# Kernel tuning notes

Measured on AMD Instinct MI355X. Metric: run time of the kernel, lower is better.

Reference implementation:

```python
import jax, jax.numpy as jnp
import numpy as np

B, D, H, W = 16, 96, 96, 96
NUM_POINTS = 4096
THRESH = 0.5
CH = [3, 64, 128, 256, 512]   # shared-MLP channel progression (3 mlp layers + global_dim)
GROUPS = 8
EPS = 1e-5
HEAD_HIDDEN = 128


def setup_inputs() -> dict:
    key = jax.random.key(0)
    ks = jax.random.split(key, 8)
    inp = {"volume": jax.random.uniform(ks[0], (B, 1, D, H, W), jnp.float32)}
    for i in range(4):
        # Conv1d(kernel=1, no bias) weight (out, in); kaiming normal fan_out -> std=sqrt(2/out)
        inp[f"w{i+1}"] = jax.random.normal(ks[1 + i], (CH[i + 1], CH[i]), jnp.float32) * np.sqrt(2.0 / CH[i + 1]).astype(np.float32)
        inp[f"gn{i+1}_w"] = jnp.ones((CH[i + 1],), jnp.float32)
        inp[f"gn{i+1}_b"] = jnp.zeros((CH[i + 1],), jnp.float32)
    inp["fc1_w"] = jax.random.normal(ks[5], (HEAD_HIDDEN, CH[-1]), jnp.float32) * np.sqrt(2.0 / HEAD_HIDDEN).astype(np.float32)
    inp["fc1_b"] = jnp.zeros((HEAD_HIDDEN,), jnp.float32)
    inp["fc2_w"] = jax.random.normal(ks[6], (1, HEAD_HIDDEN), jnp.float32) * np.sqrt(2.0).astype(np.float32)
    inp["fc2_b"] = jnp.zeros((1,), jnp.float32)
    return inp


def volume_to_points(volume):
    """Batched, jit-safe version of volume_to_pointcloud (eval mode: linspace sampling)."""
    b, _, d, h, w = volume.shape
    mask = (volume[:, 0] > THRESH).reshape(b, -1)              # (B, D*H*W)
    n = mask.sum(axis=1)                                        # (B,) foreground counts
    # Stable argsort on ~mask puts foreground flat-indices first, in ascending order
    # == torch nonzero() ordering (row-major over D,H,W).
    order = jnp.argsort(jnp.logical_not(mask), axis=1, stable=True)  # (B, D*H*W)
    p = jnp.arange(NUM_POINTS)
    n_f = n.astype(jnp.float32)[:, None]
    # torch.linspace(0, n-1, P).long(): truncation toward zero
    lin = (p[None, :].astype(jnp.float32) * (n_f - 1.0) / (NUM_POINTS - 1)).astype(jnp.int32)
    lin = jnp.clip(lin, 0, jnp.maximum(n[:, None] - 1, 0))
    wrap = p[None, :] % jnp.maximum(n[:, None], 1)              # n < P fallback
    idx = jnp.where(n[:, None] >= NUM_POINTS, lin, wrap)        # (B, P)
    flat = jnp.take_along_axis(order, idx, axis=1)              # (B, P) flat voxel indices
    dd = flat // (h * w)
    hh = (flat // w) % h
    ww = flat % w
    coords = jnp.stack([dd, hh, ww], axis=1).astype(jnp.float32)  # (B, 3, P)
    scale = jnp.array([max(d - 1, 1), max(h - 1, 1), max(w - 1, 1)], jnp.float32)
    pts = coords / scale[None, :, None] * 2.0 - 1.0
    return jnp.where((n > 0)[:, None, None], pts, 0.0)


def group_norm(x, gamma, beta):
    b, c, npts = x.shape
    xg = x.reshape(b, GROUPS, c // GROUPS, npts)
    mu = xg.mean(axis=(2, 3), keepdims=True)
    var = xg.var(axis=(2, 3), keepdims=True)
    xn = ((xg - mu) * jax.lax.rsqrt(var + EPS)).reshape(b, c, npts)
    return xn * gamma[None, :, None] + beta[None, :, None]


def reference(volume, w1, gn1_w, gn1_b, w2, gn2_w, gn2_b, w3, gn3_w, gn3_b,
              w4, gn4_w, gn4_b, fc1_w, fc1_b, fc2_w, fc2_b):
    x = volume_to_points(volume)                                 # (B, 3, P)
    for cw, gw, gb in ((w1, gn1_w, gn1_b), (w2, gn2_w, gn2_b),
                       (w3, gn3_w, gn3_b), (w4, gn4_w, gn4_b)):
        x = jax.nn.relu(group_norm(jnp.einsum('oc,bcn->bon', cw, x), gw, gb))
    g = x.max(axis=2)                                            # (B, 512) global max-pool
    hdn = jax.nn.relu(g @ fc1_w.T + fc1_b)                       # dropout is identity in eval
    logits = (hdn @ fc2_w.T + fc2_b)[:, 0]                       # squeeze(-1) -> (B,)
    return logits
```

## Files before the change

### kernel.cpp

```cpp
#include <hip/hip_runtime.h>
#include <hip/hip_bf16.h>

#define NB 16
#define VOX 884736
#define NPTS 4096
#define CHUNK 1024
#define NCHUNK 864

typedef _Float16 f16x8 __attribute__((ext_vector_type(8)));
typedef _Float16 f16x4 __attribute__((ext_vector_type(4)));
typedef float f32x4 __attribute__((ext_vector_type(4)));


__global__ __launch_bounds__(256) void count_kernel(const float* __restrict__ vol,
                                                    int* __restrict__ counts,
                                                    unsigned long long* __restrict__ bits) {
    int blk = blockIdx.x;
    const float4* v4 = (const float4*)(vol + (size_t)blk * CHUNK);
    float4 v = v4[threadIdx.x];
    int nib = (v.x > 0.5f) | ((v.y > 0.5f) << 1) | ((v.z > 0.5f) << 2) | ((v.w > 0.5f) << 3);
    __shared__ unsigned char nibs[256];
    nibs[threadIdx.x] = (unsigned char)nib;
    int cnt = __popc(nib);
    for (int off = 32; off; off >>= 1) cnt += __shfl_down(cnt, off, 64);
    __shared__ int s[4];
    if ((threadIdx.x & 63) == 0) s[threadIdx.x >> 6] = cnt;
    __syncthreads();
    if (threadIdx.x < 16) {
        unsigned long long wd = 0;
        #pragma unroll
        for (int i = 0; i < 16; i++)
            wd |= (unsigned long long)nibs[threadIdx.x * 16 + i] << (4 * i);
        bits[(size_t)blk * 16 + threadIdx.x] = wd;
    }
    if (threadIdx.x == 0) counts[blk] = s[0] + s[1] + s[2] + s[3];
}

__global__ __launch_bounds__(1024) void scan_kernel(const int* __restrict__ counts,
                                                    int* __restrict__ prefix,
                                                    int* __restrict__ totals) {
    __shared__ int s[1024];
    int b = blockIdx.x, t = threadIdx.x;
    int v = (t < NCHUNK) ? counts[b * NCHUNK + t] : 0;
    s[t] = v;
    __syncthreads();
    for (int off = 1; off < 1024; off <<= 1) {
        int x = (t >= off) ? s[t - off] : 0;
        __syncthreads();
        s[t] += x;
        __syncthreads();
    }
    if (t < NCHUNK) prefix[b * NCHUNK + t] = s[t] - v;
    if (t == NCHUNK - 1) totals[b] = s[t];
}


__global__ __launch_bounds__(256) void points_kernel(const unsigned long long* __restrict__ bits,
                                                     const int* __restrict__ prefix,
                                                     const int* __restrict__ totals,
                                                     const float* __restrict__ w1,
                                                     float* __restrict__ pts,
                                                     float* __restrict__ pstat1) {
    int b = blockIdx.x >> 4;
    int pc = blockIdx.x & 15;
    int p = pc * 256 + threadIdx.x;
    __shared__ int spref[NCHUNK];
    __shared__ float sw1[192];
    for (int i = threadIdx.x; i < NCHUNK; i += 256) spref[i] = prefix[b * NCHUNK + i];
    if (threadIdx.x < 192) sw1[threadIdx.x] = w1[threadIdx.x];
    __syncthreads();
    int n = totals[b];
    float px = 0.f, py = 0.f, pz = 0.f;
    if (n > 0) {
        int k;
        if (n >= NPTS) {
            float t = (float)p * ((float)n - 1.0f);
            t = t / 4095.0f;
            k = (int)t;
            if (k > n - 1) k = n - 1;
            if (k < 0) k = 0;
        } else {
            k = p % n;
        }
        int lo = 0, hi = NCHUNK - 1;
        while (lo < hi) {
            int mid = (lo + hi + 1) >> 1;
            if (spref[mid] <= k) lo = mid; else hi = mid - 1;
        }
        int rr = k - spref[lo];
        const unsigned long long* wb = bits + ((size_t)b * NCHUNK + lo) * 16;
        unsigned long long chosen = 0;
        int wordidx = 0;
        bool found = false;
        #pragma unroll
        for (int w = 0; w < 16; w++) {
            unsigned long long m = wb[w];
            int pcnt = __popcll(m);
            bool take = (!found) && (rr < pcnt);
            if (take) { chosen = m; wordidx = w; found = true; }
            if (!found) rr -= pcnt;
        }
        int pos = 0;
        unsigned long long m64 = chosen;
        int c = __popcll(m64 & 0xFFFFFFFFull);
        if (rr >= c) { pos = 32; rr -= c; m64 >>= 32; }
        unsigned mm = (unsigned)m64;
        c = __popc(mm & 0xFFFFu); if (rr >= c) { pos += 16; rr -= c; mm >>= 16; }
        c = __popc(mm & 0xFFu);   if (rr >= c) { pos += 8;  rr -= c; mm >>= 8; }
        c = __popc(mm & 0xFu);    if (rr >= c) { pos += 4;  rr -= c; mm >>= 4; }
        c = __popc(mm & 0x3u);    if (rr >= c) { pos += 2;  rr -= c; mm >>= 2; }
        c = mm & 1u;              if (rr >= c) { pos += 1; }
        int flat = lo * CHUNK + wordidx * 64 + pos;
        int dd = flat / 9216;
        int rem = flat - dd * 9216;
        int hh = rem / 96;
        int ww = rem - hh * 96;
        px = (float)dd / 95.0f * 2.0f - 1.0f;
        py = (float)hh / 95.0f * 2.0f - 1.0f;
        pz = (float)ww / 95.0f * 2.0f - 1.0f;
    }
    pts[((size_t)b * 3 + 0) * NPTS + p] = px;
    pts[((size_t)b * 3 + 1) * NPTS + p] = py;
    pts[((size_t)b * 3 + 2) * NPTS + p] = pz;
    float s[8] = {}, q[8] = {};
    #pragma unroll
    for (int o = 0; o < 64; o++) {
        float a = sw1[o * 3 + 0] * px + sw1[o * 3 + 1] * py + sw1[o * 3 + 2] * pz;
        s[o >> 3] += a;
        q[o >> 3] += a * a;
    }
    __shared__ float red[4][8][2];
    int wv = threadIdx.x >> 6;
    #pragma unroll
    for (int g = 0; g < 8; g++) {
        float S = s[g], Q = q[g];
        for (int off = 32; off; off >>= 1) {
            S += __shfl_down(S, off, 64);
            Q += __shfl_down(Q, off, 64);
        }
        if ((threadIdx.x & 63) == 0) { red[wv][g][0] = S; red[wv][g][1] = Q; }
    }
    __syncthreads();
    if (threadIdx.x < 8) {
        int g = threadIdx.x;
        float S = red[0][g][0] + red[1][g][0] + red[2][g][0] + red[3][g][0];
        float Q = red[0][g][1] + red[1][g][1] + red[2][g][1] + red[3][g][1];
        float* d = pstat1 + (((size_t)(b * 8 + g)) * 16 + pc) * 2;
        d[0] = S; d[1] = Q;
    }
}

__global__ __launch_bounds__(64) void gn_finalize1(const float* __restrict__ pstat,
                                                   const float* __restrict__ gamma,
                                                   const float* __restrict__ beta,
                                                   float* __restrict__ scale,
                                                   float* __restrict__ shift) {
    int b = blockIdx.x >> 3, g = blockIdx.x & 7;
    const float* base = pstat + (size_t)(b * 8 + g) * 32;
    float S = 0.f, Q = 0.f;
    if (threadIdx.x < 16) { S = base[threadIdx.x * 2]; Q = base[threadIdx.x * 2 + 1]; }
    for (int off = 8; off; off >>= 1) {
        S += __shfl_down(S, off, 64);
        Q += __shfl_down(Q, off, 64);
    }
    __shared__ float ms[2];
    if (threadIdx.x == 0) {
        float inv = 1.0f / (8.0f * 4096.0f);
        float mu = S * inv;
        float var = Q * inv - mu * mu;
        if (var < 0.f) var = 0.f;
        ms[0] = mu; ms[1] = rsqrtf(var + 1e-5f);
    }
    __syncthreads();
    if (threadIdx.x < 8) {
        int c = g * 8 + threadIdx.x;
        float ga = gamma[c] * ms[1];
        scale[b * 64 + c] = ga;
        shift[b * 64 + c] = beta[c] - ms[0] * ga;
    }
}


__device__ inline void cast_chunk(const float* __restrict__ wf, _Float16* __restrict__ wh,
                                  int CIN, int t) {
    int lane = t & 63;
    int NCB = CIN / 32;
    int cb = (t >> 6) % NCB;
    int ob = t / (64 * NCB);
    int o = ob * 16 + (lane & 15);
    int c0 = cb * 32 + (lane >> 4) * 8;
    const float* src = wf + (size_t)o * CIN + c0;
    f16x8 v;
    #pragma unroll
    for (int e = 0; e < 8; e++) v[e] = (_Float16)src[e];
    *(f16x8*)(wh + (size_t)t * 8) = v;
}

__global__ __launch_bounds__(256) void cast_w_all(const float* __restrict__ w2,
                                                  const float* __restrict__ w3,
                                                  const float* __restrict__ w4,
                                                  _Float16* __restrict__ w2f,
                                                  _Float16* __restrict__ w3f,
                                                  _Float16* __restrict__ w4f) {
    int t = blockIdx.x * 256 + threadIdx.x;
    if (t < 1024) cast_chunk(w2, w2f, 64, t);
    else if (t < 1024 + 4096) cast_chunk(w3, w3f, 128, t - 1024);
    else if (t < 1024 + 4096 + 16384) cast_chunk(w4, w4f, 256, t - 5120);
}


template <int CIN, int COUT, bool POOL>
__device__ __forceinline__ void gemm_core(const _Float16* __restrict__ sl,
                                          const _Float16* __restrict__ wfrag,
                                          _Float16* __restrict__ yout,
                                          float* __restrict__ pstat,
                                          int b, int pblk, int tid) {
    constexpr int NCB = CIN / 32;
    constexpr int SLOT = CIN / 8 - 1;
    constexpr int OFW = COUT / 32;
    constexpr int COF = OFW > 4 ? 4 : OFW;
    constexpr int NCHK = OFW / COF;
    int wv = tid >> 6, lane = tid & 63, lr = lane & 15, lk = lane >> 4;
    int ph = wv & 1, oh = wv >> 1;
    int Pg = b * 64 + pblk;
    int pb32 = (Pg << 1) | ph;
    #pragma unroll
    for (int ck = 0; ck < NCHK; ck++) {
        f32x4 acc[2][COF] = {};
        for (int cb = 0; cb < NCB; cb++) {
            int ch = cb * 4 + lk;
            f16x8 af[2];
            #pragma unroll
            for (int pf = 0; pf < 2; pf++) {
                int p = ph * 32 + pf * 16 + lr;
                af[pf] = *(const f16x8*)(sl + p * CIN + ((ch ^ (p & SLOT)) << 3));
            }
            f16x8 bf[COF];
            #pragma unroll
            for (int i = 0; i < COF; i++) {
                int ofr = oh * OFW + ck * COF + i;
                bf[i] = *(const f16x8*)(wfrag + ((size_t)(ofr * NCB + cb) * 64 + lane) * 8);
            }
            #pragma unroll
            for (int pf = 0; pf < 2; pf++)
                #pragma unroll
                for (int i = 0; i < COF; i++)
                    acc[pf][i] = __builtin_amdgcn_mfma_f32_16x16x32_f16(af[pf], bf[i], acc[pf][i], 0, 0, 0);
        }
        #pragma unroll
        for (int i = 0; i < COF; i++) {
            int ofr = oh * OFW + ck * COF + i;
            if (!POOL) {
                _Float16* ytO = yout + ((size_t)Pg * (COUT / 64) + (ofr >> 2)) * 4096;
                #pragma unroll
                for (int pf = 0; pf < 2; pf++) {
                    f16x4 vv;
                    #pragma unroll
                    for (int j = 0; j < 4; j++) vv[j] = (_Float16)acc[pf][i][j];
                    *(f16x4*)(ytO + (((ofr & 3) * 4 + ph * 2 + pf) * 64 + lane) * 4) = vv;
                }
            }
            float S = 0.f, Q = 0.f, MX = -1e30f, MN = 1e30f;
            #pragma unroll
            for (int pf = 0; pf < 2; pf++)
                #pragma unroll
                for (int j = 0; j < 4; j++) {
                    float v = acc[pf][i][j];
                    S += v; Q += v * v;
                    if (POOL) { MX = fmaxf(MX, v); MN = fminf(MN, v); }
                }
            S += __shfl_xor(S, 16, 64); Q += __shfl_xor(Q, 16, 64);
            S += __shfl_xor(S, 32, 64); Q += __shfl_xor(Q, 32, 64);
            if (POOL) {
                MX = fmaxf(MX, __shfl_xor(MX, 16, 64)); MN = fminf(MN, __shfl_xor(MN, 16, 64));
                MX = fmaxf(MX, __shfl_xor(MX, 32, 64)); MN = fminf(MN, __shfl_xor(MN, 32, 64));
            }
            if (lk == 0) {
                int o = ofr * 16 + lr;
                if (POOL) {
                    *(float4*)(pstat + ((size_t)pb32 * COUT + o) * 4) = make_float4(S, Q, MX, MN);
                } else {
                    float* d = pstat + ((size_t)pb32 * COUT + o) * 2;
                    d[0] = S; d[1] = Q;
                }
            }
        }
    }
}


__global__ __launch_bounds__(256, 4) void fused_l2(const float* __restrict__ pts,
                                                   const float* __restrict__ w1,
                                                   const float* __restrict__ scale,
                                                   const float* __restrict__ shift,
                                                   const _Float16* __restrict__ wfrag,
                                                   _Float16* __restrict__ yout,
                                                   float* __restrict__ pstat) {
    __shared__ _Float16 sl[64 * 64];
    __shared__ float sw1[192], ssc[64], ssh[64];
    int b = blockIdx.y, pblk = blockIdx.x, tid = threadIdx.x;
    if (tid < 192) sw1[tid] = w1[tid];
    if (tid < 64) { ssc[tid] = scale[b * 64 + tid]; ssh[tid] = shift[b * 64 + tid]; }
    __syncthreads();
    {
        int p = tid >> 2, qo = (tid & 3) * 16;
        int pg = pblk * 64 + p;
        float x0 = pts[((size_t)b * 3 + 0) * NPTS + pg];
        float x1 = pts[((size_t)b * 3 + 1) * NPTS + pg];
        float x2 = pts[((size_t)b * 3 + 2) * NPTS + pg];
        #pragma unroll
        for (int e = 0; e < 16; e++) {
            int o = qo + e;
            float a = sw1[o * 3 + 0] * x0 + sw1[o * 3 + 1] * x1 + sw1[o * 3 + 2] * x2;
            float r = fmaxf(a * ssc[o] + ssh[o], 0.f);
            sl[p * 64 + (((o >> 3) ^ (p & 7)) << 3) + (o & 7)] = (_Float16)r;
        }
    }
    __syncthreads();
    gemm_core<64, 128, false>(sl, wfrag, yout, pstat, b, pblk, tid);
}


template <int CIN, int COUT, bool POOL>
__global__ __launch_bounds__(256, 4) void fused_layer(const _Float16* __restrict__ yprev,
                                                      const float* __restrict__ scale,
                                                      const float* __restrict__ shift,
                                                      const _Float16* __restrict__ wfrag,
                                                      _Float16* __restrict__ yout,
                                                      float* __restrict__ pstat) {
    constexpr int SLOT = CIN / 8 - 1;
    __shared__ _Float16 sl[64 * CIN];
    __shared__ float ssc[CIN], ssh[CIN];
    int b = blockIdx.y, pblk = blockIdx.x, tid = threadIdx.x;
    int Pg = b * 64 + pblk;
    for (int i = tid; i < CIN; i += 256) { ssc[i] = scale[b * CIN + i]; ssh[i] = shift[b * CIN + i]; }
    __syncthreads();
    const _Float16* yt = yprev + (size_t)Pg * 64 * CIN;
    constexpr int NCH4 = 64 * CIN / 4;
    for (int q = tid; q < NCH4; q += 256) {
        int lane = q & 63;
        int pf = (q >> 6) & 3;
        int ofi = (q >> 8) & 3;
        int Ob = q >> 10;
        int o = Ob * 64 + ofi * 16 + (lane & 15);
        int pbase = pf * 16 + (lane >> 4) * 4;
        f16x4 v = *(const f16x4*)(yt + (size_t)q * 4);
        float sc = ssc[o], sh = ssh[o];
        int ch = o >> 3;
        #pragma unroll
        for (int e = 0; e < 4; e++) {
            int p = pbase + e;
            float r = fmaxf((float)v[e] * sc + sh, 0.f);
            sl[p * CIN + ((ch ^ (p & SLOT)) << 3) + (o & 7)] = (_Float16)r;
        }
    }
    __syncthreads();
    gemm_core<CIN, COUT, POOL>(sl, wfrag, yout, pstat, b, pblk, tid);
}


template <int C>
__global__ __launch_bounds__(256) void gn_finalizeG(const float* __restrict__ pstat,
                                                    const float* __restrict__ gamma,
                                                    const float* __restrict__ beta,
                                                    float* __restrict__ scale,
                                                    float* __restrict__ shift) {
    constexpr int GS = C / 8;
    int b = blockIdx.x >> 3, g = blockIdx.x & 7;
    const float* base = pstat + (size_t)b * 128 * C * 2;
    float S = 0.f, Q = 0.f;
    for (int i = threadIdx.x; i < 128 * GS; i += 256) {
        int pb = i / GS;
        int c = g * GS + (i % GS);
        const float* d = base + ((size_t)pb * C + c) * 2;
        S += d[0]; Q += d[1];
    }
    for (int off = 32; off; off >>= 1) {
        S += __shfl_down(S, off, 64);
        Q += __shfl_down(Q, off, 64);
    }
    __shared__ float ss[8];
    if ((threadIdx.x & 63) == 0) {
        ss[(threadIdx.x >> 6) * 2] = S;
        ss[(threadIdx.x >> 6) * 2 + 1] = Q;
    }
    __syncthreads();
    __shared__ float ms[2];
    if (threadIdx.x == 0) {
        float St = ss[0] + ss[2] + ss[4] + ss[6];
        float Qt = ss[1] + ss[3] + ss[5] + ss[7];
        float inv = 1.0f / ((float)GS * 4096.0f);
        float mu = St * inv;
        float var = Qt * inv - mu * mu;
        if (var < 0.f) var = 0.f;
        ms[0] = mu; ms[1] = rsqrtf(var + 1e-5f);
    }
    __syncthreads();
    for (int i = threadIdx.x; i < GS; i += 256) {
        int c = g * GS + i;
        float ga = gamma[c] * ms[1];
        scale[(size_t)b * C + c] = ga;
        shift[(size_t)b * C + c] = beta[c] - ms[0] * ga;
    }
}


__global__ __launch_bounds__(64) void pool_final(const float* __restrict__ pstat4,
                                                 const float* __restrict__ gamma,
                                                 const float* __restrict__ beta,
                                                 float* __restrict__ g) {
    int b = blockIdx.x >> 3, gr = blockIdx.x & 7;
    int o = gr * 64 + threadIdx.x;
    float S = 0.f, Q = 0.f, MX = -1e30f, MN = 1e30f;
    for (int pb = 0; pb < 128; pb++) {
        float4 v = *(const float4*)(pstat4 + (((size_t)(b * 128 + pb)) * 512 + o) * 4);
        S += v.x; Q += v.y; MX = fmaxf(MX, v.z); MN = fminf(MN, v.w);
    }
    float St = S, Qt = Q;
    for (int off = 32; off; off >>= 1) {
        St += __shfl_xor(St, off, 64);
        Qt += __shfl_xor(Qt, off, 64);
    }
    float inv = 1.0f / (64.0f * 4096.0f);
    float mu = St * inv;
    float var = Qt * inv - mu * mu;
    if (var < 0.f) var = 0.f;
    float rstd = rsqrtf(var + 1e-5f);
    float sc = gamma[o] * rstd;
    float sh = beta[o] - mu * sc;
    float m = (sc >= 0.f ? MX : MN) * sc + sh;
    g[b * 512 + o] = fmaxf(m, 0.f);
}


__global__ __launch_bounds__(128) void head_kernel(const float* __restrict__ g,
                                                   const float* __restrict__ fc1w,
                                                   const float* __restrict__ fc1b,
                                                   const float* __restrict__ fc2w,
                                                   const float* __restrict__ fc2b,
                                                   float* __restrict__ out) {
    int b = blockIdx.x;
    int o = threadIdx.x;
    __shared__ float sg[512];
    for (int i = threadIdx.x; i < 512; i += 128) sg[i] = g[b * 512 + i];
    __syncthreads();
    float acc = fc1b[o];
    for (int c = 0; c < 512; c++) acc += sg[c] * fc1w[o * 512 + c];
    float h = fmaxf(acc, 0.f) * fc2w[o];
    for (int off = 32; off; off >>= 1) h += __shfl_down(h, off, 64);
    __shared__ float s2[2];
    if ((threadIdx.x & 63) == 0) s2[threadIdx.x >> 6] = h;
    __syncthreads();
    if (threadIdx.x == 0) out[b] = s2[0] + s2[1] + fc2b[0];
}


extern "C" void kernel_launch(void* const* d_in, const int* in_sizes, int n_in,
                              void* d_out, int out_size, void* d_ws, size_t ws_size,
                              hipStream_t stream) {
    const float* vol  = (const float*)d_in[0];
    const float* w1   = (const float*)d_in[1];
    const float* gn1w = (const float*)d_in[2];
    const float* gn1b = (const float*)d_in[3];
    const float* w2   = (const float*)d_in[4];
    const float* gn2w = (const float*)d_in[5];
    const float* gn2b = (const float*)d_in[6];
    const float* w3   = (const float*)d_in[7];
    const float* gn3w = (const float*)d_in[8];
    const float* gn3b = (const float*)d_in[9];
    const float* w4   = (const float*)d_in[10];
    const float* gn4w = (const float*)d_in[11];
    const float* gn4b = (const float*)d_in[12];
    const float* fc1w = (const float*)d_in[13];
    const float* fc1b = (const float*)d_in[14];
    const float* fc2w = (const float*)d_in[15];
    const float* fc2b = (const float*)d_in[16];
    float* out = (float*)d_out;

    char* ws = (char*)d_ws;
    size_t cur = 0;
    auto alloc = [&](size_t bytes) -> void* {
        cur = (cur + 255) & ~(size_t)255;
        void* p = ws + cur;
        cur += bytes;
        return p;
    };
    int*      counts  = (int*)alloc((size_t)NB * NCHUNK * 4);
    int*      prefix  = (int*)alloc((size_t)NB * NCHUNK * 4);
    int*      totals  = (int*)alloc(64);
    unsigned long long* bits = (unsigned long long*)alloc((size_t)NB * NCHUNK * 16 * 8);
    float*    pts     = (float*)alloc((size_t)NB * 3 * NPTS * 4);
    float*    gbuf    = (float*)alloc((size_t)NB * 512 * 4);
    float*    pstat1  = (float*)alloc((size_t)NB * 8 * 16 * 2 * 4);
    float*    pstatG  = (float*)alloc((size_t)NB * 128 * 256 * 2 * 4);
    float*    pstat4  = (float*)alloc((size_t)NB * 128 * 512 * 4 * 4);
    float*    scale   = (float*)alloc((size_t)NB * 512 * 4);
    float*    shift   = (float*)alloc((size_t)NB * 512 * 4);
    _Float16* w2f     = (_Float16*)alloc((size_t)128 * 64 * 2);
    _Float16* w3f     = (_Float16*)alloc((size_t)256 * 128 * 2);
    _Float16* w4f     = (_Float16*)alloc((size_t)512 * 256 * 2);
    _Float16* y2      = (_Float16*)alloc((size_t)NB * NPTS * 128 * 2);
    _Float16* y3      = (_Float16*)alloc((size_t)NB * NPTS * 256 * 2);

    count_kernel<<<dim3(NB * NCHUNK), dim3(256), 0, stream>>>(vol, counts, bits);
    scan_kernel<<<dim3(NB), dim3(1024), 0, stream>>>(counts, prefix, totals);
    points_kernel<<<dim3(NB * 16), dim3(256), 0, stream>>>(bits, prefix, totals, w1, pts, pstat1);

    cast_w_all<<<dim3(84), dim3(256), 0, stream>>>(w2, w3, w4, w2f, w3f, w4f);

    gn_finalize1<<<dim3(NB * 8), dim3(64), 0, stream>>>(pstat1, gn1w, gn1b, scale, shift);
    fused_l2<<<dim3(64, NB), dim3(256), 0, stream>>>(pts, w1, scale, shift, w2f, y2, pstatG);

    gn_finalizeG<128><<<dim3(NB * 8), dim3(256), 0, stream>>>(pstatG, gn2w, gn2b, scale, shift);
    fused_layer<128, 256, false><<<dim3(64, NB), dim3(256), 0, stream>>>(y2, scale, shift, w3f, y3, pstatG);

    gn_finalizeG<256><<<dim3(NB * 8), dim3(256), 0, stream>>>(pstatG, gn3w, gn3b, scale, shift);
    fused_layer<256, 512, true><<<dim3(64, NB), dim3(256), 0, stream>>>(y3, scale, shift, w4f, nullptr, pstat4);

    pool_final<<<dim3(NB * 8), dim3(64), 0, stream>>>(pstat4, gn4w, gn4b, gbuf);
    head_kernel<<<dim3(NB), dim3(128), 0, stream>>>(gbuf, fc1w, fc1b, fc2w, fc2b, out);
}
```

Before: 122.6 us.

## Split layer-4 output channels across grid z, double-buffer MFMA loads, widen pool reduction

The final 256->512 layer is split over a third grid dimension so each block computes 256 output channels, doubling block count for better occupancy. This costs a second staging and normalisation pass of the input tile per block. The GEMM inner loop now double-buffers A/B fragment loads to overlap memory latency with MFMA issue. The tile staging loop reads 8 halves per thread instead of 4. pool_final now uses 256 threads with a shared-memory partial reduction over point blocks.

```diff
diff --git a/kernel.cpp b/kernel.cpp
--- a/kernel.cpp
+++ b/kernel.cpp
@@ -209,55 +209,64 @@
 }
 
 
-template <int CIN, int COUT, bool POOL>
+template <int CIN, int COUT, int COUT_BLK, bool POOL>
 __device__ __forceinline__ void gemm_core(const _Float16* __restrict__ sl,
-                                          const _Float16* __restrict__ wfrag,
+                                          const _Float16* __restrict__ wblk,
                                           _Float16* __restrict__ yout,
                                           float* __restrict__ pstat,
-                                          int b, int pblk, int tid) {
+                                          int b, int pblk, int obase, int tid) {
     constexpr int NCB = CIN / 32;
     constexpr int SLOT = CIN / 8 - 1;
-    constexpr int OFW = COUT / 32;
+    constexpr int OFW = COUT_BLK / 32;
     constexpr int COF = OFW > 4 ? 4 : OFW;
     constexpr int NCHK = OFW / COF;
     int wv = tid >> 6, lane = tid & 63, lr = lane & 15, lk = lane >> 4;
     int ph = wv & 1, oh = wv >> 1;
     int Pg = b * 64 + pblk;
     int pb32 = (Pg << 1) | ph;
+
+#define LOADP(CB, AF, BF)                                                               \
+    {                                                                                   \
+        int ch_ = (CB) * 4 + lk;                                                        \
+        _Pragma("unroll") for (int pf = 0; pf < 2; pf++) {                              \
+            int p_ = ph * 32 + pf * 16 + lr;                                            \
+            AF[pf] = *(const f16x8*)(sl + p_ * CIN + ((ch_ ^ (p_ & SLOT)) << 3));       \
+        }                                                                               \
+        _Pragma("unroll") for (int i_ = 0; i_ < COF; i_++) {                            \
+            int ofr_ = oh * OFW + ck * COF + i_;                                        \
+            BF[i_] = *(const f16x8*)(wblk + ((size_t)(ofr_ * NCB + (CB)) * 64 + lane) * 8); \
+        }                                                                               \
+    }
+#define MFMAP(AF, BF)                                                                   \
+    _Pragma("unroll") for (int pf = 0; pf < 2; pf++)                                    \
+        _Pragma("unroll") for (int i_ = 0; i_ < COF; i_++)                              \
+            acc[pf][i_] = __builtin_amdgcn_mfma_f32_16x16x32_f16(AF[pf], BF[i_], acc[pf][i_], 0, 0, 0);
+
     #pragma unroll
     for (int ck = 0; ck < NCHK; ck++) {
         f32x4 acc[2][COF] = {};
-        for (int cb = 0; cb < NCB; cb++) {
-            int ch = cb * 4 + lk;
-            f16x8 af[2];
-            #pragma unroll
-            for (int pf = 0; pf < 2; pf++) {
-                int p = ph * 32 + pf * 16 + lr;
-                af[pf] = *(const f16x8*)(sl + p * CIN + ((ch ^ (p & SLOT)) << 3));
-            }
-            f16x8 bf[COF];
-            #pragma unroll
-            for (int i = 0; i < COF; i++) {
-                int ofr = oh * OFW + ck * COF + i;
-                bf[i] = *(const f16x8*)(wfrag + ((size_t)(ofr * NCB + cb) * 64 + lane) * 8);
-            }
-            #pragma unroll
-            for (int pf = 0; pf < 2; pf++)
-                #pragma unroll
-                for (int i = 0; i < COF; i++)
-                    acc[pf][i] = __builtin_amdgcn_mfma_f32_16x16x32_f16(af[pf], bf[i], acc[pf][i], 0, 0, 0);
+        f16x8 af0[2], bf0[COF], af1[2], bf1[COF];
+        LOADP(0, af0, bf0)
+        LOADP(1, af1, bf1)
+        #pragma unroll
+        for (int cb = 0; cb < NCB; cb += 2) {
+            MFMAP(af0, bf0)
+            if (cb + 2 < NCB) LOADP(cb + 2, af0, bf0)
+            MFMAP(af1, bf1)
+            if (cb + 3 < NCB) LOADP(cb + 3, af1, bf1)
         }
         #pragma unroll
         for (int i = 0; i < COF; i++) {
             int ofr = oh * OFW + ck * COF + i;
+            int ofg = (obase >> 4) + ofr;
             if (!POOL) {
-                _Float16* ytO = yout + ((size_t)Pg * (COUT / 64) + (ofr >> 2)) * 4096;
+                _Float16* ytO = yout + ((size_t)Pg * (COUT / 64) + (ofg >> 2)) * 4096;
                 #pragma unroll
                 for (int pf = 0; pf < 2; pf++) {
                     f16x4 vv;
                     #pragma unroll
                     for (int j = 0; j < 4; j++) vv[j] = (_Float16)acc[pf][i][j];
-                    *(f16x4*)(ytO + (((ofr & 3) * 4 + ph * 2 + pf) * 64 + lane) * 4) = vv;
+                    *(f16x4*)(ytO + (((ofg & 3) * 4 + ph * 2 + pf) * 64 + lane) * 4) = vv;
                 }
             }
             float S = 0.f, Q = 0.f, MX = -1e30f, MN = 1e30f;
@@ -276,7 +285,7 @@
                 MX = fmaxf(MX, __shfl_xor(MX, 32, 64)); MN = fminf(MN, __shfl_xor(MN, 32, 64));
             }
             if (lk == 0) {
-                int o = ofr * 16 + lr;
+                int o = obase + ofr * 16 + lr;
                 if (POOL) {
                     *(float4*)(pstat + ((size_t)pb32 * COUT + o) * 4) = make_float4(S, Q, MX, MN);
                 } else {
@@ -286,6 +295,8 @@
             }
         }
     }
+#undef LOADP
+#undef MFMAP
 }
 
 
@@ -317,11 +328,11 @@
         }
     }
     __syncthreads();
-    gemm_core<64, 128, false>(sl, wfrag, yout, pstat, b, pblk, tid);
-}
-
-
-template <int CIN, int COUT, bool POOL>
+    gemm_core<64, 128, 128, false>(sl, wfrag, yout, pstat, b, pblk, 0, tid);
+}
+
+
+template <int CIN, int COUT, int COUT_BLK, bool POOL>
 __global__ __launch_bounds__(256, 4) void fused_layer(const _Float16* __restrict__ yprev,
                                                       const float* __restrict__ scale,
                                                       const float* __restrict__ shift,
@@ -332,30 +343,38 @@
     __shared__ _Float16 sl[64 * CIN];
     __shared__ float ssc[CIN], ssh[CIN];
     int b = blockIdx.y, pblk = blockIdx.x, tid = threadIdx.x;
+    int obase = blockIdx.z * COUT_BLK;
     int Pg = b * 64 + pblk;
     for (int i = tid; i < CIN; i += 256) { ssc[i] = scale[b * CIN + i]; ssh[i] = shift[b * CIN + i]; }
     __syncthreads();
     const _Float16* yt = yprev + (size_t)Pg * 64 * CIN;
-    constexpr int NCH4 = 64 * CIN / 4;
-    for (int q = tid; q < NCH4; q += 256) {
-        int lane = q & 63;
+    constexpr int NCH8 = 64 * CIN / 8;
+    #pragma unroll 2
+    for (int q8 = tid; q8 < NCH8; q8 += 256) {
+        int q = q8 * 2;
+        int lane0 = q & 63;
         int pf = (q >> 6) & 3;
         int ofi = (q >> 8) & 3;
         int Ob = q >> 10;
-        int o = Ob * 64 + ofi * 16 + (lane & 15);
-        int pbase = pf * 16 + (lane >> 4) * 4;
-        f16x4 v = *(const f16x4*)(yt + (size_t)q * 4);
-        float sc = ssc[o], sh = ssh[o];
-        int ch = o >> 3;
+        f16x8 v = *(const f16x8*)(yt + (size_t)q8 * 8);
         #pragma unroll
-        for (int e = 0; e < 4; e++) {
-            int p = pbase + e;
-            float r = fmaxf((float)v[e] * sc + sh, 0.f);
-            sl[p * CIN + ((ch ^ (p & SLOT)) << 3) + (o & 7)] = (_Float16)r;
-        }
-    }
-    __syncthreads();
-    gemm_core<CIN, COUT, POOL>(sl, wfrag, yout, pstat, b, pblk, tid);
+        for (int hf = 0; hf < 2; hf++) {
+            int ln = lane0 + hf;
+            int o = Ob * 64 + ofi * 16 + (ln & 15);
+            int pbase = pf * 16 + (ln >> 4) * 4;
+            float sc = ssc[o], sh = ssh[o];
+            int ch = o >> 3;
+            #pragma unroll
+            for (int e = 0; e < 4; e++) {
+                int p = pbase + e;
+                float r = fmaxf((float)v[hf * 4 + e] * sc + sh, 0.f);
+                sl[p * CIN + ((ch ^ (p & SLOT)) << 3) + (o & 7)] = (_Float16)r;
+            }
+        }
+    }
+    __syncthreads();
+    gemm_core<CIN, COUT, COUT_BLK, POOL>(sl, wfrag + (size_t)obase * CIN, yout, pstat,
+                                         b, pblk, obase, tid);
 }
 
 
@@ -405,31 +424,42 @@
 }
 
 
-__global__ __launch_bounds__(64) void pool_final(const float* __restrict__ pstat4,
-                                                 const float* __restrict__ gamma,
-                                                 const float* __restrict__ beta,
-                                                 float* __restrict__ g) {
+__global__ __launch_bounds__(256) void pool_final(const float* __restrict__ pstat4,
+                                                  const float* __restrict__ gamma,
+                                                  const float* __restrict__ beta,
+                                                  float* __restrict__ g) {
     int b = blockIdx.x >> 3, gr = blockIdx.x & 7;
-    int o = gr * 64 + threadIdx.x;
+    int ch = threadIdx.x & 63;
+    int pg = threadIdx.x >> 6;
+    int o = gr * 64 + ch;
     float S = 0.f, Q = 0.f, MX = -1e30f, MN = 1e30f;
-    for (int pb = 0; pb < 128; pb++) {
+    for (int pb = pg; pb < 128; pb += 4) {
         float4 v = *(const float4*)(pstat4 + (((size_t)(b * 128 + pb)) * 512 + o) * 4);
         S += v.x; Q += v.y; MX = fmaxf(MX, v.z); MN = fminf(MN, v.w);
     }
-    float St = S, Qt = Q;
-    for (int off = 32; off; off >>= 1) {
-        St += __shfl_xor(St, off, 64);
-        Qt += __shfl_xor(Qt, off, 64);
-    }
-    float inv = 1.0f / (64.0f * 4096.0f);
-    float mu = St * inv;
-    float var = Qt * inv - mu * mu;
-    if (var < 0.f) var = 0.f;
-    float rstd = rsqrtf(var + 1e-5f);
-    float sc = gamma[o] * rstd;
-    float sh = beta[o] - mu * sc;
-    float m = (sc >= 0.f ? MX : MN) * sc + sh;
-    g[b * 512 + o] = fmaxf(m, 0.f);
+    __shared__ float sS[4][64], sQ[4][64], sMX[4][64], sMN[4][64];
+    sS[pg][ch] = S; sQ[pg][ch] = Q; sMX[pg][ch] = MX; sMN[pg][ch] = MN;
+    __syncthreads();
+    if (threadIdx.x < 64) {
+        float Sc = sS[0][ch] + sS[1][ch] + sS[2][ch] + sS[3][ch];
+        float Qc = sQ[0][ch] + sQ[1][ch] + sQ[2][ch] + sQ[3][ch];
+        float MXc = fmaxf(fmaxf(sMX[0][ch], sMX[1][ch]), fmaxf(sMX[2][ch], sMX[3][ch]));
+        float MNc = fminf(fminf(sMN[0][ch], sMN[1][ch]), fminf(sMN[2][ch], sMN[3][ch]));
+        float St = Sc, Qt = Qc;
+        for (int off = 32; off; off >>= 1) {
+            St += __shfl_xor(St, off, 64);
+            Qt += __shfl_xor(Qt, off, 64);
+        }
+        float inv = 1.0f / (64.0f * 4096.0f);
+        float mu = St * inv;
+        float var = Qt * inv - mu * mu;
+        if (var < 0.f) var = 0.f;
+        float rstd = rsqrtf(var + 1e-5f);
+        float sc = gamma[o] * rstd;
+        float sh = beta[o] - mu * sc;
+        float m = (sc >= 0.f ? MXc : MNc) * sc + sh;
+        g[b * 512 + o] = fmaxf(m, 0.f);
+    }
 }
 
 
@@ -512,11 +542,11 @@
     fused_l2<<<dim3(64, NB), dim3(256), 0, stream>>>(pts, w1, scale, shift, w2f, y2, pstatG);
 
     gn_finalizeG<128><<<dim3(NB * 8), dim3(256), 0, stream>>>(pstatG, gn2w, gn2b, scale, shift);
-    fused_layer<128, 256, false><<<dim3(64, NB), dim3(256), 0, stream>>>(y2, scale, shift, w3f, y3, pstatG);
+    fused_layer<128, 256, 256, false><<<dim3(64, NB, 1), dim3(256), 0, stream>>>(y2, scale, shift, w3f, y3, pstatG);
 
     gn_finalizeG<256><<<dim3(NB * 8), dim3(256), 0, stream>>>(pstatG, gn3w, gn3b, scale, shift);
-    fused_layer<256, 512, true><<<dim3(64, NB), dim3(256), 0, stream>>>(y3, scale, shift, w4f, nullptr, pstat4);
-
-    pool_final<<<dim3(NB * 8), dim3(64), 0, stream>>>(pstat4, gn4w, gn4b, gbuf);
+    fused_layer<256, 512, 256, true><<<dim3(64, NB, 2), dim3(256), 0, stream>>>(y3, scale, shift, w4f, nullptr, pstat4);
+
+    pool_final<<<dim3(NB * 8), dim3(256), 0, stream>>>(pstat4, gn4w, gn4b, gbuf);
     head_kernel<<<dim3(NB), dim3(128), 0, stream>>>(gbuf, fc1w, fc1b, fc2w, fc2b, out);
 }
```

Measured after the change: 124.8 us. About the same (+1.9%).

## Store activations in MFMA fragment layout and normalize directly in registers

Applied to the files above, without the earlier changes.

Layers 2-4 now write intermediate activations in the exact per-lane MFMA operand layout. The next layer loads its A fragments straight from global memory and applies the fp16 GroupNorm scale/shift plus ReLU in registers, so the LDS staging pass and its barriers are gone. Layer 4 is split across a third grid dimension to double parallelism. pool_final now uses 256 threads and reduces the per-block stats in shared memory. The trade-off is that normalization now runs in fp16, which adds rounding error.

```diff
diff --git a/kernel.cpp b/kernel.cpp
--- a/kernel.cpp
+++ b/kernel.cpp
@@ -10,6 +10,13 @@
 typedef _Float16 f16x8 __attribute__((ext_vector_type(8)));
 typedef _Float16 f16x4 __attribute__((ext_vector_type(4)));
 typedef float f32x4 __attribute__((ext_vector_type(4)));
+
+__device__ __forceinline__ f16x8 nrelu(f16x8 y, f16x8 sc, f16x8 sh) {
+    f16x8 r = y * sc + sh;
+    #pragma unroll
+    for (int e = 0; e < 8; e++) r[e] = (r[e] > (_Float16)0.f) ? r[e] : (_Float16)0.f;
+    return r;
+}
 
 
 __global__ __launch_bounds__(256) void count_kernel(const float* __restrict__ vol,
@@ -209,92 +216,12 @@
 }
 
 
-template <int CIN, int COUT, bool POOL>
-__device__ __forceinline__ void gemm_core(const _Float16* __restrict__ sl,
-                                          const _Float16* __restrict__ wfrag,
-                                          _Float16* __restrict__ yout,
-                                          float* __restrict__ pstat,
-                                          int b, int pblk, int tid) {
-    constexpr int NCB = CIN / 32;
-    constexpr int SLOT = CIN / 8 - 1;
-    constexpr int OFW = COUT / 32;
-    constexpr int COF = OFW > 4 ? 4 : OFW;
-    constexpr int NCHK = OFW / COF;
-    int wv = tid >> 6, lane = tid & 63, lr = lane & 15, lk = lane >> 4;
-    int ph = wv & 1, oh = wv >> 1;
-    int Pg = b * 64 + pblk;
-    int pb32 = (Pg << 1) | ph;
-    #pragma unroll
-    for (int ck = 0; ck < NCHK; ck++) {
-        f32x4 acc[2][COF] = {};
-        for (int cb = 0; cb < NCB; cb++) {
-            int ch = cb * 4 + lk;
-            f16x8 af[2];
-            #pragma unroll
-            for (int pf = 0; pf < 2; pf++) {
-                int p = ph * 32 + pf * 16 + lr;
-                af[pf] = *(const f16x8*)(sl + p * CIN + ((ch ^ (p & SLOT)) << 3));
-            }
-            f16x8 bf[COF];
-            #pragma unroll
-            for (int i = 0; i < COF; i++) {
-                int ofr = oh * OFW + ck * COF + i;
-                bf[i] = *(const f16x8*)(wfrag + ((size_t)(ofr * NCB + cb) * 64 + lane) * 8);
-            }
-            #pragma unroll
-            for (int pf = 0; pf < 2; pf++)
-                #pragma unroll
-                for (int i = 0; i < COF; i++)
-                    acc[pf][i] = __builtin_amdgcn_mfma_f32_16x16x32_f16(af[pf], bf[i], acc[pf][i], 0, 0, 0);
-        }
-        #pragma unroll
-        for (int i = 0; i < COF; i++) {
-            int ofr = oh * OFW + ck * COF + i;
-            if (!POOL) {
-                _Float16* ytO = yout + ((size_t)Pg * (COUT / 64) + (ofr >> 2)) * 4096;
-                #pragma unroll
-                for (int pf = 0; pf < 2; pf++) {
-                    f16x4 vv;
-                    #pragma unroll
-                    for (int j = 0; j < 4; j++) vv[j] = (_Float16)acc[pf][i][j];
-                    *(f16x4*)(ytO + (((ofr & 3) * 4 + ph * 2 + pf) * 64 + lane) * 4) = vv;
-                }
-            }
-            float S = 0.f, Q = 0.f, MX = -1e30f, MN = 1e30f;
-            #pragma unroll
-            for (int pf = 0; pf < 2; pf++)
-                #pragma unroll
-                for (int j = 0; j < 4; j++) {
-                    float v = acc[pf][i][j];
-                    S += v; Q += v * v;
-                    if (POOL) { MX = fmaxf(MX, v); MN = fminf(MN, v); }
-                }
-            S += __shfl_xor(S, 16, 64); Q += __shfl_xor(Q, 16, 64);
-            S += __shfl_xor(S, 32, 64); Q += __shfl_xor(Q, 32, 64);
-            if (POOL) {
-                MX = fmaxf(MX, __shfl_xor(MX, 16, 64)); MN = fminf(MN, __shfl_xor(MN, 16, 64));
-                MX = fmaxf(MX, __shfl_xor(MX, 32, 64)); MN = fminf(MN, __shfl_xor(MN, 32, 64));
-            }
-            if (lk == 0) {
-                int o = ofr * 16 + lr;
-                if (POOL) {
-                    *(float4*)(pstat + ((size_t)pb32 * COUT + o) * 4) = make_float4(S, Q, MX, MN);
-                } else {
-                    float* d = pstat + ((size_t)pb32 * COUT + o) * 2;
-                    d[0] = S; d[1] = Q;
-                }
-            }
-        }
-    }
-}
-
-
 __global__ __launch_bounds__(256, 4) void fused_l2(const float* __restrict__ pts,
                                                    const float* __restrict__ w1,
                                                    const float* __restrict__ scale,
                                                    const float* __restrict__ shift,
                                                    const _Float16* __restrict__ wfrag,
-                                                   _Float16* __restrict__ yout,
+                                                   _Float16* __restrict__ y2,
                                                    float* __restrict__ pstat) {
     __shared__ _Float16 sl[64 * 64];
     __shared__ float sw1[192], ssc[64], ssh[64];
@@ -317,45 +244,190 @@
         }
     }
     __syncthreads();
-    gemm_core<64, 128, false>(sl, wfrag, yout, pstat, b, pblk, tid);
-}
-
-
-template <int CIN, int COUT, bool POOL>
-__global__ __launch_bounds__(256, 4) void fused_layer(const _Float16* __restrict__ yprev,
-                                                      const float* __restrict__ scale,
-                                                      const float* __restrict__ shift,
-                                                      const _Float16* __restrict__ wfrag,
-                                                      _Float16* __restrict__ yout,
-                                                      float* __restrict__ pstat) {
-    constexpr int SLOT = CIN / 8 - 1;
-    __shared__ _Float16 sl[64 * CIN];
-    __shared__ float ssc[CIN], ssh[CIN];
+    int wv = tid >> 6, lane = tid & 63, lr = lane & 15, lk = lane >> 4;
+    int ph = wv & 1, oh = wv >> 1;
+    int Pg = b * 64 + pblk;
+    int pb32 = (Pg << 1) | ph;
+    int P16 = Pg * 4 + ph * 2;
+    f32x4 acc[2][4] = {};
+    #pragma unroll
+    for (int cb = 0; cb < 2; cb++) {
+        int ch = cb * 4 + lk;
+        f16x8 af0, af1;
+        {
+            int p0 = ph * 32 + lr;
+            af0 = *(const f16x8*)(sl + p0 * 64 + ((ch ^ (p0 & 7)) << 3));
+            int p1 = p0 + 16;
+            af1 = *(const f16x8*)(sl + p1 * 64 + ((ch ^ (p1 & 7)) << 3));
+        }
+        #pragma unroll
+        for (int i = 0; i < 4; i++) {
+            int ofr = oh * 4 + i;
+            f16x8 bf = *(const f16x8*)(wfrag + (((size_t)ofr * 2 + cb) * 64 + lane) * 8);
+            acc[0][i] = __builtin_amdgcn_mfma_f32_16x16x32_f16(bf, af0, acc[0][i], 0, 0, 0);
+            acc[1][i] = __builtin_amdgcn_mfma_f32_16x16x32_f16(bf, af1, acc[1][i], 0, 0, 0);
+        }
+    }
+    #pragma unroll
+    for (int i = 0; i < 4; i++) {
+        int ofr = oh * 4 + i;
+        int cb2 = ofr >> 1;
+        int kg = (ofr & 1) * 2 + (lk >> 1);
+        int lanep = lr + 16 * kg;
+        int sub = lk & 1;
+        #pragma unroll
+        for (int pf = 0; pf < 2; pf++) {
+            f16x4 vv;
+            #pragma unroll
+            for (int j = 0; j < 4; j++) vv[j] = (_Float16)acc[pf][i][j];
+            *(f16x4*)(y2 + (((size_t)(P16 + pf) * 4 + cb2) * 64 + lanep) * 8 + sub * 4) = vv;
+        }
+        float s[4], q[4];
+        #pragma unroll
+        for (int j = 0; j < 4; j++) {
+            float a0 = acc[0][i][j], a1 = acc[1][i][j];
+            s[j] = a0 + a1; q[j] = a0 * a0 + a1 * a1;
+        }
+        #pragma unroll
+        for (int m = 1; m <= 8; m <<= 1)
+            #pragma unroll
+            for (int j = 0; j < 4; j++) {
+                s[j] += __shfl_xor(s[j], m, 64);
+                q[j] += __shfl_xor(q[j], m, 64);
+            }
+        if (lr == 0) {
+            int o0 = ofr * 16 + lk * 4;
+            float* d = pstat + ((size_t)pb32 * 128 + o0) * 2;
+            *(float4*)d = make_float4(s[0], q[0], s[1], q[1]);
+            *(float4*)(d + 4) = make_float4(s[2], q[2], s[3], q[3]);
+        }
+    }
+}
+
+
+__global__ __launch_bounds__(256, 4) void fused_l3(const _Float16* __restrict__ y2,
+                                                   const _Float16* __restrict__ sch2,
+                                                   const _Float16* __restrict__ shh2,
+                                                   const _Float16* __restrict__ w3f,
+                                                   _Float16* __restrict__ y3,
+                                                   float* __restrict__ pstat) {
     int b = blockIdx.y, pblk = blockIdx.x, tid = threadIdx.x;
+    int wv = tid >> 6, lane = tid & 63, lr = lane & 15, lk = lane >> 4;
+    int ph = wv & 1, oh = wv >> 1;
     int Pg = b * 64 + pblk;
-    for (int i = tid; i < CIN; i += 256) { ssc[i] = scale[b * CIN + i]; ssh[i] = shift[b * CIN + i]; }
-    __syncthreads();
-    const _Float16* yt = yprev + (size_t)Pg * 64 * CIN;
-    constexpr int NCH4 = 64 * CIN / 4;
-    for (int q = tid; q < NCH4; q += 256) {
-        int lane = q & 63;
-        int pf = (q >> 6) & 3;
-        int ofi = (q >> 8) & 3;
-        int Ob = q >> 10;
-        int o = Ob * 64 + ofi * 16 + (lane & 15);
-        int pbase = pf * 16 + (lane >> 4) * 4;
-        f16x4 v = *(const f16x4*)(yt + (size_t)q * 4);
-        float sc = ssc[o], sh = ssh[o];
-        int ch = o >> 3;
-        #pragma unroll
-        for (int e = 0; e < 4; e++) {
-            int p = pbase + e;
-            float r = fmaxf((float)v[e] * sc + sh, 0.f);
-            sl[p * CIN + ((ch ^ (p & SLOT)) << 3) + (o & 7)] = (_Float16)r;
-        }
-    }
-    __syncthreads();
-    gemm_core<CIN, COUT, POOL>(sl, wfrag, yout, pstat, b, pblk, tid);
+    int pb32 = (Pg << 1) | ph;
+    int P16 = Pg * 4 + ph * 2;
+    const _Float16* sch = sch2 + b * 128;
+    const _Float16* shh = shh2 + b * 128;
+    #pragma unroll
+    for (int ck = 0; ck < 2; ck++) {
+        f32x4 acc[2][4] = {};
+        #pragma unroll
+        for (int cb = 0; cb < 4; cb++) {
+            f16x8 scv = *(const f16x8*)(sch + cb * 32 + lk * 8);
+            f16x8 shv = *(const f16x8*)(shh + cb * 32 + lk * 8);
+            f16x8 af0 = nrelu(*(const f16x8*)(y2 + (((size_t)(P16 + 0) * 4 + cb) * 64 + lane) * 8), scv, shv);
+            f16x8 af1 = nrelu(*(const f16x8*)(y2 + (((size_t)(P16 + 1) * 4 + cb) * 64 + lane) * 8), scv, shv);
+            #pragma unroll
+            for (int i = 0; i < 4; i++) {
+                int ofr = oh * 8 + ck * 4 + i;
+                f16x8 bf = *(const f16x8*)(w3f + (((size_t)ofr * 4 + cb) * 64 + lane) * 8);
+                acc[0][i] = __builtin_amdgcn_mfma_f32_16x16x32_f16(bf, af0, acc[0][i], 0, 0, 0);
+                acc[1][i] = __builtin_amdgcn_mfma_f32_16x16x32_f16(bf, af1, acc[1][i], 0, 0, 0);
+            }
+        }
+        #pragma unroll
+        for (int i = 0; i < 4; i++) {
+            int ofr = oh * 8 + ck * 4 + i;
+            int cb3 = ofr >> 1;
+            int kg = (ofr & 1) * 2 + (lk >> 1);
+            int lanep = lr + 16 * kg;
+            int sub = lk & 1;
+            #pragma unroll
+            for (int pf = 0; pf < 2; pf++) {
+                f16x4 vv;
+                #pragma unroll
+                for (int j = 0; j < 4; j++) vv[j] = (_Float16)acc[pf][i][j];
+                *(f16x4*)(y3 + (((size_t)(P16 + pf) * 8 + cb3) * 64 + lanep) * 8 + sub * 4) = vv;
+            }
+            float s[4], q[4];
+            #pragma unroll
+            for (int j = 0; j < 4; j++) {
+                float a0 = acc[0][i][j], a1 = acc[1][i][j];
+                s[j] = a0 + a1; q[j] = a0 * a0 + a1 * a1;
+            }
+            #pragma unroll
+            for (int m = 1; m <= 8; m <<= 1)
+                #pragma unroll
+                for (int j = 0; j < 4; j++) {
+                    s[j] += __shfl_xor(s[j], m, 64);
+                    q[j] += __shfl_xor(q[j], m, 64);
+                }
+            if (lr == 0) {
+                int o0 = ofr * 16 + lk * 4;
+                float* d = pstat + ((size_t)pb32 * 256 + o0) * 2;
+                *(float4*)d = make_float4(s[0], q[0], s[1], q[1]);
+                *(float4*)(d + 4) = make_float4(s[2], q[2], s[3], q[3]);
+            }
+        }
+    }
+}
+
+
+__global__ __launch_bounds__(256, 4) void fused_l4(const _Float16* __restrict__ y3,
+                                                   const _Float16* __restrict__ sch3,
+                                                   const _Float16* __restrict__ shh3,
+                                                   const _Float16* __restrict__ w4f,
+                                                   float* __restrict__ pstat4) {
+    int b = blockIdx.y, pblk = blockIdx.x, tid = threadIdx.x;
+    int obase = blockIdx.z * 256;
+    int wv = tid >> 6, lane = tid & 63, lr = lane & 15, lk = lane >> 4;
+    int ph = wv & 1, oh = wv >> 1;
+    int Pg = b * 64 + pblk;
+    int pb32 = (Pg << 1) | ph;
+    int P16 = Pg * 4 + ph * 2;
+    const _Float16* sch = sch3 + b * 256;
+    const _Float16* shh = shh3 + b * 256;
+    const _Float16* wblk = w4f + (size_t)obase * 256;
+    #pragma unroll
+    for (int ck = 0; ck < 2; ck++) {
+        f32x4 acc[2][4] = {};
+        #pragma unroll
+        for (int cb = 0; cb < 8; cb++) {
+            f16x8 scv = *(const f16x8*)(sch + cb * 32 + lk * 8);
+            f16x8 shv = *(const f16x8*)(shh + cb * 32 + lk * 8);
+            f16x8 af0 = nrelu(*(const f16x8*)(y3 + (((size_t)(P16 + 0) * 8 + cb) * 64 + lane) * 8), scv, shv);
+            f16x8 af1 = nrelu(*(const f16x8*)(y3 + (((size_t)(P16 + 1) * 8 + cb) * 64 + lane) * 8), scv, shv);
+            #pragma unroll
+            for (int i = 0; i < 4; i++) {
+                int ofr = oh * 8 + ck * 4 + i;
+                f16x8 bf = *(const f16x8*)(wblk + (((size_t)ofr * 8 + cb) * 64 + lane) * 8);
+                acc[0][i] = __builtin_amdgcn_mfma_f32_16x16x32_f16(af0, bf, acc[0][i], 0, 0, 0);
+                acc[1][i] = __builtin_amdgcn_mfma_f32_16x16x32_f16(af1, bf, acc[1][i], 0, 0, 0);
+            }
+        }
+        #pragma unroll
+        for (int i = 0; i < 4; i++) {
+            int ofr = oh * 8 + ck * 4 + i;
+            float S = 0.f, Q = 0.f, MX = -1e30f, MN = 1e30f;
+            #pragma unroll
+            for (int pf = 0; pf < 2; pf++)
+                #pragma unroll
+                for (int j = 0; j < 4; j++) {
+                    float v = acc[pf][i][j];
+                    S += v; Q += v * v;
+                    MX = fmaxf(MX, v); MN = fminf(MN, v);
+                }
+            S += __shfl_xor(S, 16, 64); Q += __shfl_xor(Q, 16, 64);
+            MX = fmaxf(MX, __shfl_xor(MX, 16, 64)); MN = fminf(MN, __shfl_xor(MN, 16, 64));
+            S += __shfl_xor(S, 32, 64); Q += __shfl_xor(Q, 32, 64);
+            MX = fmaxf(MX, __shfl_xor(MX, 32, 64)); MN = fminf(MN, __shfl_xor(MN, 32, 64));
+            if (lk == 0) {
+                int o = obase + ofr * 16 + lr;
+                *(float4*)(pstat4 + ((size_t)pb32 * 512 + o) * 4) = make_float4(S, Q, MX, MN);
+            }
+        }
+    }
 }
 
 
@@ -363,8 +435,8 @@
 __global__ __launch_bounds__(256) void gn_finalizeG(const float* __restrict__ pstat,
                                                     const float* __restrict__ gamma,
                                                     const float* __restrict__ beta,
-                                                    float* __restrict__ scale,
-                                                    float* __restrict__ shift) {
+                                                    _Float16* __restrict__ scaleh,
+                                                    _Float16* __restrict__ shifth) {
     constexpr int GS = C / 8;
     int b = blockIdx.x >> 3, g = blockIdx.x & 7;
     const float* base = pstat + (size_t)b * 128 * C * 2;
@@ -399,37 +471,48 @@
     for (int i = threadIdx.x; i < GS; i += 256) {
         int c = g * GS + i;
         float ga = gamma[c] * ms[1];
-        scale[(size_t)b * C + c] = ga;
-        shift[(size_t)b * C + c] = beta[c] - ms[0] * ga;
-    }
-}
-
-
-__global__ __launch_bounds__(64) void pool_final(const float* __restrict__ pstat4,
-                                                 const float* __restrict__ gamma,
-                                                 const float* __restrict__ beta,
-                                                 float* __restrict__ g) {
+        scaleh[(size_t)b * C + c] = (_Float16)ga;
+        shifth[(size_t)b * C + c] = (_Float16)(beta[c] - ms[0] * ga);
+    }
+}
+
+
+__global__ __launch_bounds__(256) void pool_final(const float* __restrict__ pstat4,
+                                                  const float* __restrict__ gamma,
+                                                  const float* __restrict__ beta,
+                                                  float* __restrict__ g) {
     int b = blockIdx.x >> 3, gr = blockIdx.x & 7;
-    int o = gr * 64 + threadIdx.x;
+    int ch = threadIdx.x & 63;
+    int pg = threadIdx.x >> 6;
+    int o = gr * 64 + ch;
     float S = 0.f, Q = 0.f, MX = -1e30f, MN = 1e30f;
-    for (int pb = 0; pb < 128; pb++) {
+    for (int pb = pg; pb < 128; pb += 4) {
         float4 v = *(const float4*)(pstat4 + (((size_t)(b * 128 + pb)) * 512 + o) * 4);
         S += v.x; Q += v.y; MX = fmaxf(MX, v.z); MN = fminf(MN, v.w);
     }
-    float St = S, Qt = Q;
-    for (int off = 32; off; off >>= 1) {
-        St += __shfl_xor(St, off, 64);
-        Qt += __shfl_xor(Qt, off, 64);
-    }
-    float inv = 1.0f / (64.0f * 4096.0f);
-    float mu = St * inv;
-    float var = Qt * inv - mu * mu;
-    if (var < 0.f) var = 0.f;
-    float rstd = rsqrtf(var + 1e-5f);
-    float sc = gamma[o] * rstd;
-    float sh = beta[o] - mu * sc;
-    float m = (sc >= 0.f ? MX : MN) * sc + sh;
-    g[b * 512 + o] = fmaxf(m, 0.f);
+    __shared__ float sS[4][64], sQ[4][64], sMX[4][64], sMN[4][64];
+    sS[pg][ch] = S; sQ[pg][ch] = Q; sMX[pg][ch] = MX; sMN[pg][ch] = MN;
+    __syncthreads();
+    if (threadIdx.x < 64) {
+        float Sc = sS[0][ch] + sS[1][ch] + sS[2][ch] + sS[3][ch];
+        float Qc = sQ[0][ch] + sQ[1][ch] + sQ[2][ch] + sQ[3][ch];
+        float MXc = fmaxf(fmaxf(sMX[0][ch], sMX[1][ch]), fmaxf(sMX[2][ch], sMX[3][ch]));
+        float MNc = fminf(fminf(sMN[0][ch], sMN[1][ch]), fminf(sMN[2][ch], sMN[3][ch]));
+        float St = Sc, Qt = Qc;
+        for (int off = 32; off; off >>= 1) {
+            St += __shfl_xor(St, off, 64);
+            Qt += __shfl_xor(Qt, off, 64);
+        }
+        float inv = 1.0f / (64.0f * 4096.0f);
+        float mu = St * inv;
+        float var = Qt * inv - mu * mu;
+        if (var < 0.f) var = 0.f;
+        float rstd = rsqrtf(var + 1e-5f);
+        float sc = gamma[o] * rstd;
+        float sh = beta[o] - mu * sc;
+        float m = (sc >= 0.f ? MXc : MNc) * sc + sh;
+        g[b * 512 + o] = fmaxf(m, 0.f);
+    }
 }
 
 
@@ -494,8 +577,12 @@
     float*    pstat1  = (float*)alloc((size_t)NB * 8 * 16 * 2 * 4);
     float*    pstatG  = (float*)alloc((size_t)NB * 128 * 256 * 2 * 4);
     float*    pstat4  = (float*)alloc((size_t)NB * 128 * 512 * 4 * 4);
-    float*    scale   = (float*)alloc((size_t)NB * 512 * 4);
-    float*    shift   = (float*)alloc((size_t)NB * 512 * 4);
+    float*    scale1  = (float*)alloc((size_t)NB * 64 * 4);
+    float*    shift1  = (float*)alloc((size_t)NB * 64 * 4);
+    _Float16* sc2h    = (_Float16*)alloc((size_t)NB * 128 * 2);
+    _Float16* sh2h    = (_Float16*)alloc((size_t)NB * 128 * 2);
+    _Float16* sc3h    = (_Float16*)alloc((size_t)NB * 256 * 2);
+    _Float16* sh3h    = (_Float16*)alloc((size_t)NB * 256 * 2);
     _Float16* w2f     = (_Float16*)alloc((size_t)128 * 64 * 2);
     _Float16* w3f     = (_Float16*)alloc((size_t)256 * 128 * 2);
     _Float16* w4f     = (_Float16*)alloc((size_t)512 * 256 * 2);
@@ -508,15 +595,15 @@
 
     cast_w_all<<<dim3(84), dim3(256), 0, stream>>>(w2, w3, w4, w2f, w3f, w4f);
 
-    gn_finalize1<<<dim3(NB * 8), dim3(64), 0, stream>>>(pstat1, gn1w, gn1b, scale, shift);
-    fused_l2<<<dim3(64, NB), dim3(256), 0, stream>>>(pts, w1, scale, shift, w2f, y2, pstatG);
-
-    gn_finalizeG<128><<<dim3(NB * 8), dim3(256), 0, stream>>>(pstatG, gn2w, gn2b, scale, shift);
-    fused_layer<128, 256, false><<<dim3(64, NB), dim3(256), 0, stream>>>(y2, scale, shift, w3f, y3, pstatG);
-
-    gn_finalizeG<256><<<dim3(NB * 8), dim3(256), 0, stream>>>(pstatG, gn3w, gn3b, scale, shift);
-    fused_layer<256, 512, true><<<dim3(64, NB), dim3(256), 0, stream>>>(y3, scale, shift, w4f, nullptr, pstat4);
-
-    pool_final<<<dim3(NB * 8), dim3(64), 0, stream>>>(pstat4, gn4w, gn4b, gbuf);
+    gn_finalize1<<<dim3(NB * 8), dim3(64), 0, stream>>>(pstat1, gn1w, gn1b, scale1, shift1);
+    fused_l2<<<dim3(64, NB), dim3(256), 0, stream>>>(pts, w1, scale1, shift1, w2f, y2, pstatG);
+
+    gn_finalizeG<128><<<dim3(NB * 8), dim3(256), 0, stream>>>(pstatG, gn2w, gn2b, sc2h, sh2h);
+    fused_l3<<<dim3(64, NB), dim3(256), 0, stream>>>(y2, sc2h, sh2h, w3f, y3, pstatG);
+
+    gn_finalizeG<256><<<dim3(NB * 8), dim3(256), 0, stream>>>(pstatG, gn3w, gn3b, sc3h, sh3h);
+    fused_l4<<<dim3(64, NB, 2), dim3(256), 0, stream>>>(y3, sc3h, sh3h, w4f, pstat4);
+
+    pool_final<<<dim3(NB * 8), dim3(256), 0, stream>>>(pstat4, gn4w, gn4b, gbuf);
     head_kernel<<<dim3(NB), dim3(128), 0, stream>>>(gbuf, fc1w, fc1b, fc2w, fc2b, out);
 }
```

Result: slower. 154.9 us (+26.4%).
